# Kernel optimization log

Hardware: AMD Instinct MI355X
Metric: run time of the kernel (lower is better)

Reference implementation:

```python
import jax, jax.numpy as jnp
import numpy as np

N0, N1 = 20000, 20000     # users, items
F0 = 512                  # raw feature dim per type
HID = 64                  # hidden_dim == H * D
H, D = 8, 8               # num_heads, out_dim
P = 2                     # metapaths per side
E = 200000                # metapath instances per metapath
L = 3                     # metapath length (nodes)
B = 8192                  # link-prediction target batch
AV = 128                  # attn_vec_dim
CH = 128                  # ProductMLP hidden = max(128, HID//2)
ETYPES_USER = [[0, 1], [0, 1]]
ETYPES_ITEM = [[1, 0], [1, 0]]


def setup_inputs() -> dict:
    key = jax.random.key(0)
    ks = jax.random.split(key, 32)
    def nrm(k, shape, fan_in):
        return (jax.random.normal(k, shape, dtype=jnp.float32) * (1.414 / np.sqrt(fan_in))).astype(jnp.float32)
    inp = {}
    inp['feats0'] = jax.random.normal(ks[0], (N0, F0), dtype=jnp.float32)
    inp['feats1'] = jax.random.normal(ks[1], (N1, F0), dtype=jnp.float32)
    for t, off in ((0, 2), (1, 6)):
        inp[f'tower{t}_pw'] = nrm(ks[off], (F0, HID), F0)
        inp[f'tower{t}_pb'] = jnp.zeros((HID,), jnp.float32)
        inp[f'tower{t}_w2'] = nrm(ks[off + 1], (HID, HID), HID)
        inp[f'tower{t}_b2'] = jnp.zeros((HID,), jnp.float32)
        inp[f'tower{t}_g'] = jnp.ones((HID,), jnp.float32)
        inp[f'tower{t}_be'] = jnp.zeros((HID,), jnp.float32)
    inp['r_vec'] = jax.random.normal(ks[10], (2, HID // 2, 2), dtype=jnp.float32)
    inp['attn_user'] = nrm(ks[11], (P, H, D), D)
    inp['attn_item'] = nrm(ks[12], (P, H, D), D)
    inp['su_w1'] = nrm(ks[13], (HID, AV), HID)
    inp['su_b1'] = jnp.zeros((AV,), jnp.float32)
    inp['su_w2'] = nrm(ks[14], (AV,), AV)
    inp['si_w1'] = nrm(ks[15], (HID, AV), HID)
    inp['si_b1'] = jnp.zeros((AV,), jnp.float32)
    inp['si_w2'] = nrm(ks[16], (AV,), AV)
    inp['cw1'] = nrm(ks[17], (HID, CH), HID)
    inp['cb1'] = jnp.zeros((CH,), jnp.float32)
    inp['cw2'] = nrm(ks[18], (CH, 2), CH)
    inp['idx0'] = jnp.arange(N0, dtype=jnp.int32)
    inp['idx1'] = jnp.arange(N1, dtype=jnp.int32) + N0
    inp['emi_user'] = jax.random.randint(ks[20], (P, E, L), 0, N0 + N1, dtype=jnp.int32)
    inp['tgt_user'] = jax.random.randint(ks[21], (P, E), 0, B, dtype=jnp.int32)
    inp['emi_item'] = jax.random.randint(ks[22], (P, E, L), 0, N0 + N1, dtype=jnp.int32)
    inp['tgt_item'] = jax.random.randint(ks[23], (P, E), 0, B, dtype=jnp.int32)
    return inp


def _tower(x, pw, pb, w2, b2, g, be):
    # Linear -> GELU -> Linear -> residual -> LayerNorm (dropout off in eval)
    z = x @ pw + pb
    h = jax.nn.gelu(z, approximate=False)
    h = h @ w2 + b2
    y = h + z
    mu = y.mean(-1, keepdims=True)
    var = ((y - mu) ** 2).mean(-1, keepdims=True)
    return (y - mu) / jnp.sqrt(var + 1e-5) * g + be


def _rot_full(r_vec):
    # normalize to unit complex, then even etypes = r, odd etypes = conj(r)
    r = r_vec / jnp.linalg.norm(r_vec, axis=-1, keepdims=True)
    conj = r * jnp.array([1.0, -1.0], dtype=r.dtype)
    return jnp.stack([r, conj], axis=1).reshape(-1, r.shape[1], 2)  # [num_edge_type, HID//2, 2]


def _final_r(rfull, etypes):
    # cumulative complex rotation applied to each position along the metapath
    fr = [None] * L
    fr[L - 1] = jnp.stack([jnp.ones(HID // 2), jnp.zeros(HID // 2)], axis=1).astype(rfull.dtype)
    for i in range(L - 2, -1, -1):
        rv = rfull[etypes[i]]
        re = fr[i + 1][:, 0] * rv[:, 0] - fr[i + 1][:, 1] * rv[:, 1]
        im = fr[i + 1][:, 0] * rv[:, 1] + fr[i + 1][:, 1] * rv[:, 0]
        fr[i] = jnp.stack([re, im], axis=1)
    return jnp.stack(fr)  # [L, HID//2, 2]


def _metapath(feat, emi, tgt, attn, etypes, rfull):
    # gather node features along each metapath instance: [E, L, HID//2, 2]
    ed = feat[emi].reshape(emi.shape[0], L, HID // 2, 2)
    fr = _final_r(rfull, etypes)  # last position is identity rotation
    re = ed[..., 0] * fr[:, :, 0] - ed[..., 1] * fr[:, :, 1]
    im = ed[..., 0] * fr[:, :, 1] + ed[..., 1] * fr[:, :, 0]
    hidden = jnp.stack([re, im], -1).mean(axis=1).reshape(-1, HID)  # mean over metapath positions
    eft = hidden.reshape(-1, H, D)
    e = jax.nn.leaky_relu((eft * attn).sum(-1), 0.01)  # [E, H]
    # edge softmax over instances sharing a target node
    m = jax.ops.segment_max(e, tgt, num_segments=B)
    m = jnp.where(jnp.isfinite(m), m, 0.0)
    a = jnp.exp(e - m[tgt])
    s = jax.ops.segment_sum(a, tgt, num_segments=B)
    w = a / (s[tgt] + 1e-9)
    ret = jax.ops.segment_sum(w[..., None] * eft, tgt, num_segments=B)  # [B, H, D]
    return jax.nn.elu(ret.reshape(B, HID))


def _semantic(outs, w1, b1, w2):
    hs = jnp.stack(outs)  # [P, B, HID]
    s = (jnp.tanh(hs @ w1 + b1) @ w2).mean(axis=1)  # [P]
    beta = jax.nn.softmax(s)
    return (beta[:, None, None] * hs).sum(0)  # [B, HID]


def reference(feats0, feats1, tower0_pw, tower0_pb, tower0_w2, tower0_b2, tower0_g, tower0_be,
              tower1_pw, tower1_pb, tower1_w2, tower1_b2, tower1_g, tower1_be,
              r_vec, attn_user, attn_item, su_w1, su_b1, su_w2, si_w1, si_b1, si_w2,
              cw1, cb1, cw2, idx0, idx1, emi_user, tgt_user, emi_item, tgt_item):
    t0 = _tower(feats0, tower0_pw, tower0_pb, tower0_w2, tower0_b2, tower0_g, tower0_be)
    t1 = _tower(feats1, tower1_pw, tower1_pb, tower1_w2, tower1_b2, tower1_g, tower1_be)
    feat = jnp.zeros((N0 + N1, HID), jnp.float32).at[idx0].set(t0).at[idx1].set(t1)
    rfull = _rot_full(r_vec)
    user_outs = [_metapath(feat, emi_user[p], tgt_user[p], attn_user[p], ETYPES_USER[p], rfull) for p in range(P)]
    item_outs = [_metapath(feat, emi_item[p], tgt_item[p], attn_item[p], ETYPES_ITEM[p], rfull) for p in range(P)]
    h_user = _semantic(user_outs, su_w1, su_b1, su_w2)
    h_item = _semantic(item_outs, si_w1, si_b1, si_w2)
    x = h_user * h_item
    h = jax.nn.relu(x @ cw1 + cb1)
    logits = h @ cw2
    return jax.nn.softmax(logits, axis=-1)
```

## Files before the change

kernel.cpp:

```cpp
#include <hip/hip_runtime.h>
#include <hip/hip_bf16.h>
#include <math.h>

#define NN0 20000
#define NN1 20000
#define NTOT 40000
#define FF0 512
#define HIDD 64
#define EEE 200000
#define BBB 8192
#define AVV 128
#define CHH 128

typedef __bf16 bf16x8 __attribute__((ext_vector_type(8)));
typedef __bf16 bf16x4 __attribute__((ext_vector_type(4)));
typedef float f32x4 __attribute__((ext_vector_type(4)));
typedef float f32x2 __attribute__((ext_vector_type(2)));

__device__ __forceinline__ float fast_tanh(float x) {
    float e2 = __expf(2.f * x);
    return 1.f - 2.f / (e2 + 1.f);
}

__device__ __forceinline__ f32x2 bf2_to_f32x2(unsigned int c) {
    f32x2 r;
    r.x = __uint_as_float(c << 16);
    r.y = __uint_as_float(c & 0xffff0000u);
    return r;
}

__global__ __launch_bounds__(256) void prep_hist(
    const float* __restrict__ pw0, const float* __restrict__ pw1,
    const float* __restrict__ w20, const float* __restrict__ w21,
    __bf16* __restrict__ wprep, __bf16* __restrict__ w2prep,
    const int* __restrict__ tgt_user, const int* __restrict__ tgt_item,
    int* __restrict__ cnt)
{
    int bx = blockIdx.x;
    if (bx < 16) {
        int tw = bx & 1, seg = bx >> 1;
        const float* w = tw ? pw1 : pw0;
        __bf16* base = wprep + tw * 65536;
        for (int idx = seg * 4096 + threadIdx.x; idx < (seg + 1) * 4096; idx += 256) {
            int k = idx >> 6, n = idx & 63;
            float v = w[idx];
            __bf16 hi = (__bf16)v;
            __bf16 lo = (__bf16)(v - (float)hi);
            int ks = k >> 5, kb = (k >> 3) & 3, j = k & 7;
            int nt = n >> 4, fr = n & 15;
            int lane = kb * 16 + fr;
            int off = ((ks * 4 + nt) * 64 + lane) * 8 + j;
            base[off] = hi;
            base[32768 + off] = lo;
        }
        const float* w2 = tw ? w21 : w20;
        __bf16* base2 = w2prep + tw * 8192;
        for (int idx = seg * 512 + threadIdx.x; idx < (seg + 1) * 512; idx += 256) {
            int k = idx >> 6, n = idx & 63;
            float v = w2[idx];
            __bf16 hi = (__bf16)v;
            __bf16 lo = (__bf16)(v - (float)hi);
            int ks = k >> 5, kb = (k >> 3) & 3, j = k & 7;
            int nt = n >> 4, fr = n & 15;
            int lane = kb * 16 + fr;
            int off = ((ks * 4 + nt) * 64 + lane) * 8 + j;
            base2[off] = hi;
            base2[4096 + off] = lo;
        }
    } else {
        int flat = bx - 16;
        int combo = flat & 3, blk = flat >> 2;
        const int* tgt = (combo < 2 ? tgt_user : tgt_item) + (long)(combo & 1) * EEE;
        int i = blk * 256 + threadIdx.x;
        if (i < EEE) atomicAdd(&cnt[combo * BBB + tgt[i]], 1);
    }
}

__global__ __launch_bounds__(256) void scan_kernel(const int* __restrict__ cnt, int* __restrict__ offs,
                                                   int* __restrict__ cur32, float* __restrict__ s_acc)
{
    int pth = blockIdx.x;
    if (pth == 0 && threadIdx.x < 4) s_acc[threadIdx.x] = 0.f;
    const int* c = cnt + pth * BBB;
    int* o = offs + pth * (BBB + 1);
    __shared__ int part[256];
    int tid = threadIdx.x;
    int base = tid * 32;
    int local[32];
    int sum = 0;
    for (int j = 0; j < 32; j++) { local[j] = sum; sum += c[base + j]; }
    part[tid] = sum;
    __syncthreads();
    for (int d = 1; d < 256; d <<= 1) {
        int v = (tid >= d) ? part[tid - d] : 0;
        __syncthreads();
        part[tid] += v;
        __syncthreads();
    }
    int pre = (tid == 0) ? 0 : part[tid - 1];
    for (int j = 0; j < 32; j++) {
        int val = pre + local[j];
        o[base + j] = val;
        if (((base + j) & 255) == 0) cur32[pth * 32 + ((base + j) >> 8)] = val;
    }
    if (tid == 255) o[BBB] = pre + sum;
}

#define CHUNKF 512
__global__ __launch_bounds__(64) void tower_binA(
    const float* __restrict__ x0, const float* __restrict__ x1,
    const __bf16* __restrict__ wprep, const __bf16* __restrict__ w2prep,
    const float* __restrict__ pb0, const float* __restrict__ pb1,
    const float* __restrict__ b20, const float* __restrict__ b21,
    const float* __restrict__ g0, const float* __restrict__ g1,
    const float* __restrict__ be0, const float* __restrict__ be1,
    const int* __restrict__ idxa, const int* __restrict__ idxb,
    __hip_bfloat16* __restrict__ feat,
    const int* __restrict__ tgt_user, const int* __restrict__ tgt_item,
    const int* __restrict__ emi_user, const int* __restrict__ emi_item,
    int* __restrict__ cur32, ushort4* __restrict__ binbuf)
{
    __shared__ __align__(16) char pool[4624];
    int bx = blockIdx.x;
    if (bx < 2500) {
        int tile = bx >> 1, tw = bx & 1;
        const float* x  = tw ? x1 : x0;
        const float* pb = tw ? pb1 : pb0;
        const float* b2 = tw ? b21 : b20;
        const float* g  = tw ? g1 : g0;
        const float* be = tw ? be1 : be0;
        const int* idx  = tw ? idxb : idxa;
        float (*hs)[68] = (float(*)[68])pool;

        int l = threadIdx.x;
        int fr = l & 15, kb = l >> 4;
        int row0 = tile * 16;
        const float* xp = x + (long)(row0 + fr) * FF0 + kb * 8;
        const __bf16* bp = wprep + tw * 65536;

        f32x4 acc[4];
#pragma unroll
        for (int nt = 0; nt < 4; nt++) acc[nt] = (f32x4){0.f, 0.f, 0.f, 0.f};

        float4 a0c, a1c, a0n, a1n;
        bf16x8 bhc[4], blc[4], bhn[4], bln[4];

        a0c = *(const float4*)xp;
        a1c = *(const float4*)(xp + 4);
#pragma unroll
        for (int nt = 0; nt < 4; nt++) {
            bhc[nt] = *(const bf16x8*)(bp + (nt * 64 + l) * 8);
            blc[nt] = *(const bf16x8*)(bp + 32768 + (nt * 64 + l) * 8);
        }

#pragma unroll 2
        for (int ks = 0; ks < 16; ks++) {
            if (ks + 1 < 16) {
                a0n = *(const float4*)(xp + (ks + 1) * 32);
                a1n = *(const float4*)(xp + (ks + 1) * 32 + 4);
#pragma unroll
                for (int nt = 0; nt < 4; nt++) {
                    bhn[nt] = *(const bf16x8*)(bp + (((ks + 1) * 4 + nt) * 64 + l) * 8);
                    bln[nt] = *(const bf16x8*)(bp + 32768 + (((ks + 1) * 4 + nt) * 64 + l) * 8);
                }
            }
            float av[8] = {a0c.x, a0c.y, a0c.z, a0c.w, a1c.x, a1c.y, a1c.z, a1c.w};
            bf16x8 ah, al;
#pragma unroll
            for (int j = 0; j < 8; j++) {
                __bf16 h = (__bf16)av[j];
                ah[j] = h;
                al[j] = (__bf16)(av[j] - (float)h);
            }
#pragma unroll
            for (int nt = 0; nt < 4; nt++) {
                acc[nt] = __builtin_amdgcn_mfma_f32_16x16x32_bf16(ah, bhc[nt], acc[nt], 0, 0, 0);
                acc[nt] = __builtin_amdgcn_mfma_f32_16x16x32_bf16(al, bhc[nt], acc[nt], 0, 0, 0);
                acc[nt] = __builtin_amdgcn_mfma_f32_16x16x32_bf16(ah, blc[nt], acc[nt], 0, 0, 0);
            }
            a0c = a0n; a1c = a1n;
#pragma unroll
            for (int nt = 0; nt < 4; nt++) { bhc[nt] = bhn[nt]; blc[nt] = bln[nt]; }
        }

        float pbv[4], b2v[4];
#pragma unroll
        for (int nt = 0; nt < 4; nt++) { pbv[nt] = pb[nt * 16 + fr]; b2v[nt] = b2[nt * 16 + fr]; }
        f32x4 acc2[4];
#pragma unroll
        for (int nt = 0; nt < 4; nt++) {
#pragma unroll
            for (int j = 0; j < 4; j++) {
                float z = acc[nt][j] + pbv[nt];
                float h = 0.5f * z * (1.f + erff(z * 0.70710678118654752f));
                hs[kb * 4 + j][nt * 16 + fr] = h;
                acc2[nt][j] = z + b2v[nt];
            }
        }
        __syncthreads();

        const __bf16* w2p = w2prep + tw * 8192;
#pragma unroll
        for (int ks = 0; ks < 2; ks++) {
            float4 h0 = *(const float4*)&hs[fr][ks * 32 + kb * 8];
            float4 h1 = *(const float4*)&hs[fr][ks * 32 + kb * 8 + 4];
            float hv[8] = {h0.x, h0.y, h0.z, h0.w, h1.x, h1.y, h1.z, h1.w};
            bf16x8 ah, al;
#pragma unroll
            for (int j = 0; j < 8; j++) {
                __bf16 h = (__bf16)hv[j];
                ah[j] = h;
                al[j] = (__bf16)(hv[j] - (float)h);
            }
#pragma unroll
            for (int nt = 0; nt < 4; nt++) {
                bf16x8 bh2 = *(const bf16x8*)(w2p + ((ks * 4 + nt) * 64 + l) * 8);
                bf16x8 bl2 = *(const bf16x8*)(w2p + 4096 + ((ks * 4 + nt) * 64 + l) * 8);
                acc2[nt] = __builtin_amdgcn_mfma_f32_16x16x32_bf16(ah, bh2, acc2[nt], 0, 0, 0);
                acc2[nt] = __builtin_amdgcn_mfma_f32_16x16x32_bf16(al, bh2, acc2[nt], 0, 0, 0);
                acc2[nt] = __builtin_amdgcn_mfma_f32_16x16x32_bf16(ah, bl2, acc2[nt], 0, 0, 0);
            }
        }
        __syncthreads();

        float gv[4], bev[4];
#pragma unroll
        for (int nt = 0; nt < 4; nt++) { gv[nt] = g[nt * 16 + fr]; bev[nt] = be[nt * 16 + fr]; }
#pragma unroll
        for (int j = 0; j < 4; j++) {
            float p = acc2[0][j] + acc2[1][j] + acc2[2][j] + acc2[3][j];
            p += __shfl_xor(p, 1); p += __shfl_xor(p, 2);
            p += __shfl_xor(p, 4); p += __shfl_xor(p, 8);
            float mu = p * (1.f / 64.f);
            float d[4], vs = 0.f;
#pragma unroll
            for (int nt = 0; nt < 4; nt++) { d[nt] = acc2[nt][j] - mu; vs += d[nt] * d[nt]; }
            vs += __shfl_xor(vs, 1); vs += __shfl_xor(vs, 2);
            vs += __shfl_xor(vs, 4); vs += __shfl_xor(vs, 8);
            float is = 1.f / sqrtf(vs * (1.f / 64.f) + 1e-5f);
#pragma unroll
            for (int nt = 0; nt < 4; nt++)
                hs[kb * 4 + j][nt * 16 + fr] = d[nt] * is * gv[nt] + bev[nt];
        }
        __syncthreads();
#pragma unroll 4
        for (int r = 0; r < 16; r++) {
            int grow = row0 + r;
            feat[(long)idx[grow] * HIDD + l] = __float2bfloat16(hs[r][l]);
        }
    } else {
        int flat = bx - 2500;
        int combo = flat & 3;
        int base = (flat >> 2) * CHUNKF;
        const int* tgt = (combo < 2 ? tgt_user : tgt_item) + (long)(combo & 1) * EEE;
        const int* emi = (combo < 2 ? emi_user : emi_item) + (long)(combo & 1) * EEE * 3;
        ushort4* sbuf = (ushort4*)pool;
        int* lcnt  = (int*)(pool + 4096);
        int* lofs  = lcnt + 32;
        int* gbase = lofs + 33;
        int* lcur  = gbase + 32;
        int tid = threadIdx.x;
        if (tid < 32) { lcnt[tid] = 0; lcur[tid] = 0; }
        __syncthreads();
        ushort4 ent[8]; int bk[8];
#pragma unroll
        for (int ps = 0; ps < 8; ps++) {
            int i = base + ps * 64 + tid;
            if (i < EEE) {
                int t = tgt[i];
                ent[ps] = make_ushort4((unsigned short)emi[3 * i], (unsigned short)emi[3 * i + 1],
                                       (unsigned short)emi[3 * i + 2], (unsigned short)t);
                bk[ps] = t >> 8;
                atomicAdd(&lcnt[bk[ps]], 1);
            } else bk[ps] = -1;
        }
        __syncthreads();
        if (tid == 0) {
            int run = 0;
            for (int k = 0; k < 32; k++) { lofs[k] = run; run += lcnt[k]; }
            lofs[32] = run;
        }
        __syncthreads();
        if (tid < 32) gbase[tid] = atomicAdd(&cur32[combo * 32 + tid], lcnt[tid]);
        __syncthreads();
#pragma unroll
        for (int ps = 0; ps < 8; ps++) {
            if (bk[ps] >= 0) {
                int pos = lofs[bk[ps]] + atomicAdd(&lcur[bk[ps]], 1);
                sbuf[pos] = ent[ps];
            }
        }
        __syncthreads();
        int total = lofs[32];
        ushort4* dst = binbuf + (long)combo * EEE;
        for (int j = tid; j < total; j += 64) {
            ushort4 e = sbuf[j];
            int k = e.w >> 8;
            dst[gbase[k] + (j - lofs[k])] = e;
        }
    }
}

__global__ __launch_bounds__(256) void binB_kernel(
    const int* __restrict__ offs, int* __restrict__ cur,
    const ushort4* __restrict__ binbuf, ushort4* __restrict__ nodes)
{
    int combo = blockIdx.y;
    int k = blockIdx.x >> 1, part = blockIdx.x & 1;
    const int* of = offs + combo * (BBB + 1);
    int rbeg = of[k << 8], rend = of[(k + 1) << 8];
    const ushort4* src = binbuf + (long)combo * EEE;
    ushort4* dst = nodes + (long)combo * EEE;
    int* cu = cur + combo * BBB;
    for (int j = rbeg + part * 256 + threadIdx.x; j < rend; j += 512) {
        ushort4 e = src[j];
        int t = e.w;
        int pos = of[t] + atomicAdd(&cu[t], 1);
        dst[pos] = e;
    }
}

__global__ __launch_bounds__(256) void flash_mp(
    const __hip_bfloat16* __restrict__ feat, const ushort4* __restrict__ nodes,
    const int* __restrict__ offs, const float* __restrict__ r_vec,
    const float* __restrict__ attn_user, const float* __restrict__ attn_item,
    float* __restrict__ ret)
{
    int combo = blockIdx.y;
    int wid = threadIdx.x >> 6, lane = threadIdx.x & 63;
    int half = lane >> 5, p = lane & 31;
    int side = combo >> 1;
    const float* attn = (side == 0 ? attn_user : attn_item) + (combo & 1) * 64;
    const unsigned int* f2 = (const unsigned int*)feat;
    float2 rb = ((const float2*)r_vec)[p];
    float invn = 1.f / sqrtf(rb.x * rb.x + rb.y * rb.y);
    float rvx = rb.x * invn, rvy = rb.y * invn;
    if (side == 0) rvy = -rvy;
    float aRe = attn[2 * p], aIm = attn[2 * p + 1];
    f32x2 av  = { aRe * (1.f / 3.f), aIm * (1.f / 3.f) };
    f32x2 apv = { (rvx * aRe + rvy * aIm) * (1.f / 3.f),
                  (rvx * aIm - rvy * aRe) * (1.f / 3.f) };
    int t = blockIdx.x * 4 + wid;
    const int* of = offs + combo * (BBB + 1);
    int beg = of[t], end = of[t + 1];
    int n = end - beg;
    const ushort4* nd = nodes + (long)combo * EEE;

    float m = -3.4e38f, s = 0.f;
    f32x2 A02 = {0.f, 0.f}, A1 = {0.f, 0.f};

    unsigned int c0[4], c1[4], c2[4];
    ushort4 nq[4];
    if (n > 0) {
#pragma unroll
        for (int q = 0; q < 4; q++) {
            ushort4 a = nd[min(beg + 2 * q + half, EEE - 1)];
            c0[q] = f2[(int)a.x * 32 + p];
            c1[q] = f2[(int)a.y * 32 + p];
            c2[q] = f2[(int)a.z * 32 + p];
        }
#pragma unroll
        for (int q = 0; q < 4; q++)
            nq[q] = nd[min(beg + 8 + 2 * q + half, EEE - 1)];
    }
    for (int it = 0; it < n; it += 8) {
        f32x2 u1[4], v02[4];
        float e[4];
#pragma unroll
        for (int q = 0; q < 4; q++) {
            f32x2 u0 = bf2_to_f32x2(c0[q]);
            u1[q]    = bf2_to_f32x2(c1[q]);
            f32x2 u2 = bf2_to_f32x2(c2[q]);
            v02[q] = u0 + u2;
        }
        if (it + 8 < n) {
#pragma unroll
            for (int q = 0; q < 4; q++) {
                c0[q] = f2[(int)nq[q].x * 32 + p];
                c1[q] = f2[(int)nq[q].y * 32 + p];
                c2[q] = f2[(int)nq[q].z * 32 + p];
            }
#pragma unroll
            for (int q = 0; q < 4; q++)
                nq[q] = nd[min(beg + it + 16 + 2 * q + half, EEE - 1)];
        }
#pragma unroll
        for (int q = 0; q < 4; q++) {
            f32x2 tt = v02[q] * av + u1[q] * apv;
            float pa = tt.x + tt.y;
            pa += __shfl_xor(pa, 1);
            pa += __shfl_xor(pa, 2);
            e[q] = fmaxf(pa, 0.01f * pa);
        }
        if (it + 8 > n) {
#pragma unroll
            for (int q = 0; q < 4; q++)
                if (it + 2 * q + half >= n) e[q] = -3.4e38f;
        }
        float mx = fmaxf(fmaxf(e[0], e[1]), fmaxf(e[2], e[3]));
        float mn = fmaxf(m, fmaxf(mx, __shfl_xor(mx, 32)));
        float alpha = __expf(m - mn);
        s *= alpha; A02 *= alpha; A1 *= alpha;
        float wl = 0.f;
#pragma unroll
        for (int q = 0; q < 4; q++) {
            float w = __expf(e[q] - mn);
            wl += w;
            A02 += v02[q] * w;
            A1  += u1[q] * w;
        }
        s += wl + __shfl_xor(wl, 32);
        m = mn;
    }
    float Sx = A02.x + __shfl_xor(A02.x, 32);
    float Sy = A02.y + __shfl_xor(A02.y, 32);
    float Tx = A1.x + __shfl_xor(A1.x, 32);
    float Ty = A1.y + __shfl_xor(A1.y, 32);
    float inv = (1.f / 3.f) / (s + 1e-9f);
    float vx = (Sx + rvx * Tx - rvy * Ty) * inv;
    float vy = (Sy + rvx * Ty + rvy * Tx) * inv;
    vx = vx > 0.f ? vx : __expf(vx) - 1.f;
    vy = vy > 0.f ? vy : __expf(vy) - 1.f;
    if (half == 0)
        ((float2*)ret)[((long)combo * BBB + t) * 32 + p] = make_float2(vx, vy);
}

__global__ __launch_bounds__(256) void sem_kernel(
    const float* __restrict__ ret,
    const float* __restrict__ su_w1, const float* __restrict__ su_b1, const float* __restrict__ su_w2,
    const float* __restrict__ si_w1, const float* __restrict__ si_b1, const float* __restrict__ si_w2,
    float* __restrict__ s_acc)
{
    int combo = blockIdx.y;
    int side = combo >> 1;
    const float* w1 = side ? si_w1 : su_w1;
    const float* b1 = side ? si_b1 : su_b1;
    const float* w2 = side ? si_w2 : su_w2;
    __shared__ float vs[64][68];
    __shared__ float w1s[64][128];
    int tid = threadIdx.x;
    int rowbase = blockIdx.x * 64;
    const float4* r4 = (const float4*)ret;
    for (int li = tid; li < 1024; li += 256) {
        int r = li >> 4, c4 = li & 15;
        float4 v = r4[((long)combo * BBB + rowbase + r) * 16 + c4];
        *(float4*)&vs[r][c4 * 4] = v;
    }
    const float4* w14 = (const float4*)w1;
    for (int li = tid; li < 2048; li += 256) {
        float4 v = w14[li];
        *(float4*)&w1s[li >> 5][(li & 31) * 4] = v;
    }
    __syncthreads();
    int ct = tid & 15, rt = tid >> 4;
    float acc[4][8];
#pragma unroll
    for (int cc = 0; cc < 8; cc++) {
        float b = b1[8 * ct + cc];
#pragma unroll
        for (int j = 0; j < 4; j++) acc[j][cc] = b;
    }
    for (int k = 0; k < 64; k += 4) {
        float4 xv[4];
#pragma unroll
        for (int j = 0; j < 4; j++) xv[j] = *(const float4*)&vs[4 * rt + j][k];
#pragma unroll
        for (int kk = 0; kk < 4; kk++) {
            float4 wv0 = *(const float4*)&w1s[k + kk][8 * ct];
            float4 wv1 = *(const float4*)&w1s[k + kk][8 * ct + 4];
#pragma unroll
            for (int j = 0; j < 4; j++) {
                float xx = kk == 0 ? xv[j].x : kk == 1 ? xv[j].y : kk == 2 ? xv[j].z : xv[j].w;
                acc[j][0] = fmaf(xx, wv0.x, acc[j][0]);
                acc[j][1] = fmaf(xx, wv0.y, acc[j][1]);
                acc[j][2] = fmaf(xx, wv0.z, acc[j][2]);
                acc[j][3] = fmaf(xx, wv0.w, acc[j][3]);
                acc[j][4] = fmaf(xx, wv1.x, acc[j][4]);
                acc[j][5] = fmaf(xx, wv1.y, acc[j][5]);
                acc[j][6] = fmaf(xx, wv1.z, acc[j][6]);
                acc[j][7] = fmaf(xx, wv1.w, acc[j][7]);
            }
        }
    }
    float tot = 0.f;
#pragma unroll
    for (int cc = 0; cc < 8; cc++) {
        float w2v = w2[8 * ct + cc];
#pragma unroll
        for (int j = 0; j < 4; j++) tot += fast_tanh(acc[j][cc]) * w2v;
    }
    for (int off = 32; off; off >>= 1) tot += __shfl_xor(tot, off);
    __shared__ float red[4];
    int lane = tid & 63, wid = tid >> 6;
    if (lane == 0) red[wid] = tot;
    __syncthreads();
    if (tid == 0) atomicAdd(&s_acc[combo], red[0] + red[1] + red[2] + red[3]);
}

__global__ __launch_bounds__(256) void final_kernel(
    const float* __restrict__ ret, const float* __restrict__ s_acc,
    const float* __restrict__ cw1, const float* __restrict__ cb1, const float* __restrict__ cw2,
    float* __restrict__ outp)
{
    float s0 = s_acc[0] * (1.f / BBB), s1 = s_acc[1] * (1.f / BBB);
    float s2 = s_acc[2] * (1.f / BBB), s3 = s_acc[3] * (1.f / BBB);
    float mu = fmaxf(s0, s1);
    float e0 = __expf(s0 - mu), e1 = __expf(s1 - mu);
    float bu0 = e0 / (e0 + e1), bu1 = e1 / (e0 + e1);
    float mi = fmaxf(s2, s3);
    float f0 = __expf(s2 - mi), f1 = __expf(s3 - mi);
    float bi0 = f0 / (f0 + f1), bi1 = f1 / (f0 + f1);

    __shared__ float xsld[64][68];
    __shared__ float w1s[64][128];
    int tid = threadIdx.x;
    int rowbase = blockIdx.x * 64;
    const float4* r4 = (const float4*)ret;
    for (int li = tid; li < 1024; li += 256) {
        int r = li >> 4, c4 = li & 15;
        float4 a = r4[((long)0 * BBB + rowbase + r) * 16 + c4];
        float4 b = r4[((long)1 * BBB + rowbase + r) * 16 + c4];
        float4 cc = r4[((long)2 * BBB + rowbase + r) * 16 + c4];
        float4 d = r4[((long)3 * BBB + rowbase + r) * 16 + c4];
        float4 xv;
        xv.x = (bu0 * a.x + bu1 * b.x) * (bi0 * cc.x + bi1 * d.x);
        xv.y = (bu0 * a.y + bu1 * b.y) * (bi0 * cc.y + bi1 * d.y);
        xv.z = (bu0 * a.z + bu1 * b.z) * (bi0 * cc.z + bi1 * d.z);
        xv.w = (bu0 * a.w + bu1 * b.w) * (bi0 * cc.w + bi1 * d.w);
        *(float4*)&xsld[r][c4 * 4] = xv;
    }
    const float4* w14 = (const float4*)cw1;
    for (int li = tid; li < 2048; li += 256) {
        float4 v = w14[li];
        *(float4*)&w1s[li >> 5][(li & 31) * 4] = v;
    }
    __syncthreads();
    int ct = tid & 15, rt = tid >> 4;
    float acc[4][8];
#pragma unroll
    for (int cc = 0; cc < 8; cc++) {
        float b = cb1[8 * ct + cc];
#pragma unroll
        for (int j = 0; j < 4; j++) acc[j][cc] = b;
    }
    for (int k = 0; k < 64; k += 4) {
        float4 xv[4];
#pragma unroll
        for (int j = 0; j < 4; j++) xv[j] = *(const float4*)&xsld[4 * rt + j][k];
#pragma unroll
        for (int kk = 0; kk < 4; kk++) {
            float4 wv0 = *(const float4*)&w1s[k + kk][8 * ct];
            float4 wv1 = *(const float4*)&w1s[k + kk][8 * ct + 4];
#pragma unroll
            for (int j = 0; j < 4; j++) {
                float xx = kk == 0 ? xv[j].x : kk == 1 ? xv[j].y : kk == 2 ? xv[j].z : xv[j].w;
                acc[j][0] = fmaf(xx, wv0.x, acc[j][0]);
                acc[j][1] = fmaf(xx, wv0.y, acc[j][1]);
                acc[j][2] = fmaf(xx, wv0.z, acc[j][2]);
                acc[j][3] = fmaf(xx, wv0.w, acc[j][3]);
                acc[j][4] = fmaf(xx, wv1.x, acc[j][4]);
                acc[j][5] = fmaf(xx, wv1.y, acc[j][5]);
                acc[j][6] = fmaf(xx, wv1.z, acc[j][6]);
                acc[j][7] = fmaf(xx, wv1.w, acc[j][7]);
            }
        }
    }
    float pp0[4], pp1[4];
#pragma unroll
    for (int j = 0; j < 4; j++) { pp0[j] = 0.f; pp1[j] = 0.f; }
#pragma unroll
    for (int cc = 0; cc < 8; cc++) {
        int col = 8 * ct + cc;
        float c0 = cw2[col * 2], c1 = cw2[col * 2 + 1];
#pragma unroll
        for (int j = 0; j < 4; j++) {
            float h = fmaxf(acc[j][cc], 0.f);
            pp0[j] = fmaf(h, c0, pp0[j]);
            pp1[j] = fmaf(h, c1, pp1[j]);
        }
    }
    __syncthreads();
    float2* red = (float2*)xsld;
#pragma unroll
    for (int j = 0; j < 4; j++)
        red[(4 * rt + j) * 16 + ct] = make_float2(pp0[j], pp1[j]);
    __syncthreads();
    if (tid < 64) {
        float q0 = 0.f, q1 = 0.f;
        for (int i = 0; i < 16; i++) {
            float2 e = red[tid * 16 + i];
            q0 += e.x; q1 += e.y;
        }
        float mx = fmaxf(q0, q1);
        float a0 = __expf(q0 - mx), a1 = __expf(q1 - mx);
        float dn = a0 + a1;
        outp[(rowbase + tid) * 2] = a0 / dn;
        outp[(rowbase + tid) * 2 + 1] = a1 / dn;
    }
}

extern "C" void kernel_launch(void* const* d_in, const int* in_sizes, int n_in,
                              void* d_out, int out_size, void* d_ws, size_t ws_size,
                              hipStream_t stream)
{
    const float* feats0 = (const float*)d_in[0];
    const float* feats1 = (const float*)d_in[1];
    const float* t0_pw = (const float*)d_in[2];
    const float* t0_pb = (const float*)d_in[3];
    const float* t0_w2 = (const float*)d_in[4];
    const float* t0_b2 = (const float*)d_in[5];
    const float* t0_g  = (const float*)d_in[6];
    const float* t0_be = (const float*)d_in[7];
    const float* t1_pw = (const float*)d_in[8];
    const float* t1_pb = (const float*)d_in[9];
    const float* t1_w2 = (const float*)d_in[10];
    const float* t1_b2 = (const float*)d_in[11];
    const float* t1_g  = (const float*)d_in[12];
    const float* t1_be = (const float*)d_in[13];
    const float* r_vec = (const float*)d_in[14];
    const float* attn_user = (const float*)d_in[15];
    const float* attn_item = (const float*)d_in[16];
    const float* su_w1 = (const float*)d_in[17];
    const float* su_b1 = (const float*)d_in[18];
    const float* su_w2 = (const float*)d_in[19];
    const float* si_w1 = (const float*)d_in[20];
    const float* si_b1 = (const float*)d_in[21];
    const float* si_w2 = (const float*)d_in[22];
    const float* cw1 = (const float*)d_in[23];
    const float* cb1 = (const float*)d_in[24];
    const float* cw2 = (const float*)d_in[25];
    const int* idx0 = (const int*)d_in[26];
    const int* idx1 = (const int*)d_in[27];
    const int* emi_user = (const int*)d_in[28];
    const int* tgt_user = (const int*)d_in[29];
    const int* emi_item = (const int*)d_in[30];
    const int* tgt_item = (const int*)d_in[31];
    float* outp = (float*)d_out;

    char* ws = (char*)d_ws;
    __hip_bfloat16* feat = (__hip_bfloat16*)(ws + 0);
    int*     cnt    = (int*)(ws + 5120000);
    int*     cur    = (int*)(ws + 5251072);
    int*     cur32  = (int*)(ws + 5382144);
    int*     offs   = (int*)(ws + 5382656);
    float*   s_acc  = (float*)(ws + 5513984);
    ushort4* binbuf = (ushort4*)(ws + 5514240);
    ushort4* nodes  = (ushort4*)(ws + 11914240);
    float*   ret_buf= (float*)(ws + 18314240);
    __bf16*  wprep  = (__bf16*)(ws + 26702848);
    __bf16*  w2prep = (__bf16*)(ws + 11914240);

    hipMemsetAsync(cnt, 0, 2 * 4 * BBB * sizeof(int), stream);

    prep_hist<<<16 + 4 * ((EEE + 255) / 256), 256, 0, stream>>>(
        t0_pw, t1_pw, t0_w2, t1_w2, wprep, w2prep, tgt_user, tgt_item, cnt);

    scan_kernel<<<4, 256, 0, stream>>>(cnt, offs, cur32, s_acc);

    tower_binA<<<2500 + 4 * ((EEE + CHUNKF - 1) / CHUNKF), 64, 0, stream>>>(
        feats0, feats1, wprep, w2prep, t0_pb, t1_pb,
        t0_b2, t1_b2, t0_g, t1_g, t0_be, t1_be, idx0, idx1, feat,
        tgt_user, tgt_item, emi_user, emi_item, cur32, binbuf);

    binB_kernel<<<dim3(64, 4), 256, 0, stream>>>(offs, cur, binbuf, nodes);

    flash_mp<<<dim3(BBB / 4, 4), 256, 0, stream>>>(feat, nodes, offs, r_vec,
                                                   attn_user, attn_item, ret_buf);

    sem_kernel<<<dim3(BBB / 64, 4), 256, 0, stream>>>(ret_buf, su_w1, su_b1, su_w2,
                                                      si_w1, si_b1, si_w2, s_acc);
    final_kernel<<<BBB / 64, 256, 0, stream>>>(ret_buf, s_acc, cw1, cb1, cw2, outp);
}
```

Before: 332.6 us.

## Split tower tile across two waves per block and widen binning chunks

The fused tower/binning kernel now launches 128-thread blocks. In the tower path, each wave computes half of the 64 output columns for its 16-row tile, and the LayerNorm mean and variance are combined across the two waves through shared-memory partial sums. The binning path processes 1024-entry chunks with 128 threads, so that path launches half as many blocks. The aim is more parallelism and less per-wave latency on the x-streaming GEMM. In exchange it adds extra barriers and LDS traffic, and each wave re-reads the same A rows from memory.

```diff
diff --git a/kernel.cpp b/kernel.cpp
--- a/kernel.cpp
+++ b/kernel.cpp
@@ -106,8 +106,8 @@
     if (tid == 255) o[BBB] = pre + sum;
 }
 
-#define CHUNKF 512
-__global__ __launch_bounds__(64) void tower_binA(
+#define CHUNKF 1024
+__global__ __launch_bounds__(128) void tower_binA(
     const float* __restrict__ x0, const float* __restrict__ x1,
     const __bf16* __restrict__ wprep, const __bf16* __restrict__ w2prep,
     const float* __restrict__ pb0, const float* __restrict__ pb1,
@@ -120,7 +120,7 @@
     const int* __restrict__ emi_user, const int* __restrict__ emi_item,
     int* __restrict__ cur32, ushort4* __restrict__ binbuf)
 {
-    __shared__ __align__(16) char pool[4624];
+    __shared__ __align__(16) char pool[8960];
     int bx = blockIdx.x;
     if (bx < 2500) {
         int tile = bx >> 1, tw = bx & 1;
@@ -131,26 +131,30 @@
         const float* be = tw ? be1 : be0;
         const int* idx  = tw ? idxb : idxa;
         float (*hs)[68] = (float(*)[68])pool;
-
-        int l = threadIdx.x;
+        float* pq  = (float*)(pool + 4352);
+        float* pq2 = (float*)(pool + 4480);
+
+        int wv = threadIdx.x >> 6;
+        int l = threadIdx.x & 63;
         int fr = l & 15, kb = l >> 4;
+        int nt0 = 2 * wv;
         int row0 = tile * 16;
         const float* xp = x + (long)(row0 + fr) * FF0 + kb * 8;
         const __bf16* bp = wprep + tw * 65536;
 
-        f32x4 acc[4];
-#pragma unroll
-        for (int nt = 0; nt < 4; nt++) acc[nt] = (f32x4){0.f, 0.f, 0.f, 0.f};
+        f32x4 acc[2];
+#pragma unroll
+        for (int n2 = 0; n2 < 2; n2++) acc[n2] = (f32x4){0.f, 0.f, 0.f, 0.f};
 
         float4 a0c, a1c, a0n, a1n;
-        bf16x8 bhc[4], blc[4], bhn[4], bln[4];
+        bf16x8 bhc[2], blc[2], bhn[2], bln[2];
 
         a0c = *(const float4*)xp;
         a1c = *(const float4*)(xp + 4);
 #pragma unroll
-        for (int nt = 0; nt < 4; nt++) {
-            bhc[nt] = *(const bf16x8*)(bp + (nt * 64 + l) * 8);
-            blc[nt] = *(const bf16x8*)(bp + 32768 + (nt * 64 + l) * 8);
+        for (int n2 = 0; n2 < 2; n2++) {
+            bhc[n2] = *(const bf16x8*)(bp + ((nt0 + n2) * 64 + l) * 8);
+            blc[n2] = *(const bf16x8*)(bp + 32768 + ((nt0 + n2) * 64 + l) * 8);
         }
 
 #pragma unroll 2
@@ -159,9 +163,9 @@
                 a0n = *(const float4*)(xp + (ks + 1) * 32);
                 a1n = *(const float4*)(xp + (ks + 1) * 32 + 4);
 #pragma unroll
-                for (int nt = 0; nt < 4; nt++) {
-                    bhn[nt] = *(const bf16x8*)(bp + (((ks + 1) * 4 + nt) * 64 + l) * 8);
-                    bln[nt] = *(const bf16x8*)(bp + 32768 + (((ks + 1) * 4 + nt) * 64 + l) * 8);
+                for (int n2 = 0; n2 < 2; n2++) {
+                    bhn[n2] = *(const bf16x8*)(bp + (((ks + 1) * 4 + nt0 + n2) * 64 + l) * 8);
+                    bln[n2] = *(const bf16x8*)(bp + 32768 + (((ks + 1) * 4 + nt0 + n2) * 64 + l) * 8);
                 }
             }
             float av[8] = {a0c.x, a0c.y, a0c.z, a0c.w, a1c.x, a1c.y, a1c.z, a1c.w};
@@ -173,28 +177,31 @@
                 al[j] = (__bf16)(av[j] - (float)h);
             }
 #pragma unroll
-            for (int nt = 0; nt < 4; nt++) {
-                acc[nt] = __builtin_amdgcn_mfma_f32_16x16x32_bf16(ah, bhc[nt], acc[nt], 0, 0, 0);
-                acc[nt] = __builtin_amdgcn_mfma_f32_16x16x32_bf16(al, bhc[nt], acc[nt], 0, 0, 0);
-                acc[nt] = __builtin_amdgcn_mfma_f32_16x16x32_bf16(ah, blc[nt], acc[nt], 0, 0, 0);
+            for (int n2 = 0; n2 < 2; n2++) {
+                acc[n2] = __builtin_amdgcn_mfma_f32_16x16x32_bf16(ah, bhc[n2], acc[n2], 0, 0, 0);
+                acc[n2] = __builtin_amdgcn_mfma_f32_16x16x32_bf16(al, bhc[n2], acc[n2], 0, 0, 0);
+                acc[n2] = __builtin_amdgcn_mfma_f32_16x16x32_bf16(ah, blc[n2], acc[n2], 0, 0, 0);
             }
             a0c = a0n; a1c = a1n;
 #pragma unroll
-            for (int nt = 0; nt < 4; nt++) { bhc[nt] = bhn[nt]; blc[nt] = bln[nt]; }
-        }
-
-        float pbv[4], b2v[4];
-#pragma unroll
-        for (int nt = 0; nt < 4; nt++) { pbv[nt] = pb[nt * 16 + fr]; b2v[nt] = b2[nt * 16 + fr]; }
-        f32x4 acc2[4];
-#pragma unroll
-        for (int nt = 0; nt < 4; nt++) {
+            for (int n2 = 0; n2 < 2; n2++) { bhc[n2] = bhn[n2]; blc[n2] = bln[n2]; }
+        }
+
+        float pbv[2], b2v[2];
+#pragma unroll
+        for (int n2 = 0; n2 < 2; n2++) {
+            pbv[n2] = pb[(nt0 + n2) * 16 + fr];
+            b2v[n2] = b2[(nt0 + n2) * 16 + fr];
+        }
+        f32x4 acc2[2];
+#pragma unroll
+        for (int n2 = 0; n2 < 2; n2++) {
 #pragma unroll
             for (int j = 0; j < 4; j++) {
-                float z = acc[nt][j] + pbv[nt];
+                float z = acc[n2][j] + pbv[n2];
                 float h = 0.5f * z * (1.f + erff(z * 0.70710678118654752f));
-                hs[kb * 4 + j][nt * 16 + fr] = h;
-                acc2[nt][j] = z + b2v[nt];
+                hs[kb * 4 + j][(nt0 + n2) * 16 + fr] = h;
+                acc2[n2][j] = z + b2v[n2];
             }
         }
         __syncthreads();
@@ -213,40 +220,66 @@
                 al[j] = (__bf16)(hv[j] - (float)h);
             }
 #pragma unroll
-            for (int nt = 0; nt < 4; nt++) {
-                bf16x8 bh2 = *(const bf16x8*)(w2p + ((ks * 4 + nt) * 64 + l) * 8);
-                bf16x8 bl2 = *(const bf16x8*)(w2p + 4096 + ((ks * 4 + nt) * 64 + l) * 8);
-                acc2[nt] = __builtin_amdgcn_mfma_f32_16x16x32_bf16(ah, bh2, acc2[nt], 0, 0, 0);
-                acc2[nt] = __builtin_amdgcn_mfma_f32_16x16x32_bf16(al, bh2, acc2[nt], 0, 0, 0);
-                acc2[nt] = __builtin_amdgcn_mfma_f32_16x16x32_bf16(ah, bl2, acc2[nt], 0, 0, 0);
-            }
-        }
-        __syncthreads();
-
-        float gv[4], bev[4];
-#pragma unroll
-        for (int nt = 0; nt < 4; nt++) { gv[nt] = g[nt * 16 + fr]; bev[nt] = be[nt * 16 + fr]; }
+            for (int n2 = 0; n2 < 2; n2++) {
+                bf16x8 bh2 = *(const bf16x8*)(w2p + ((ks * 4 + nt0 + n2) * 64 + l) * 8);
+                bf16x8 bl2 = *(const bf16x8*)(w2p + 4096 + ((ks * 4 + nt0 + n2) * 64 + l) * 8);
+                acc2[n2] = __builtin_amdgcn_mfma_f32_16x16x32_bf16(ah, bh2, acc2[n2], 0, 0, 0);
+                acc2[n2] = __builtin_amdgcn_mfma_f32_16x16x32_bf16(al, bh2, acc2[n2], 0, 0, 0);
+                acc2[n2] = __builtin_amdgcn_mfma_f32_16x16x32_bf16(ah, bl2, acc2[n2], 0, 0, 0);
+            }
+        }
+
+        float pj[4];
 #pragma unroll
         for (int j = 0; j < 4; j++) {
-            float p = acc2[0][j] + acc2[1][j] + acc2[2][j] + acc2[3][j];
+            float p = acc2[0][j] + acc2[1][j];
             p += __shfl_xor(p, 1); p += __shfl_xor(p, 2);
             p += __shfl_xor(p, 4); p += __shfl_xor(p, 8);
-            float mu = p * (1.f / 64.f);
-            float d[4], vs = 0.f;
-#pragma unroll
-            for (int nt = 0; nt < 4; nt++) { d[nt] = acc2[nt][j] - mu; vs += d[nt] * d[nt]; }
-            vs += __shfl_xor(vs, 1); vs += __shfl_xor(vs, 2);
-            vs += __shfl_xor(vs, 4); vs += __shfl_xor(vs, 8);
-            float is = 1.f / sqrtf(vs * (1.f / 64.f) + 1e-5f);
-#pragma unroll
-            for (int nt = 0; nt < 4; nt++)
-                hs[kb * 4 + j][nt * 16 + fr] = d[nt] * is * gv[nt] + bev[nt];
-        }
-        __syncthreads();
-#pragma unroll 4
-        for (int r = 0; r < 16; r++) {
-            int grow = row0 + r;
-            feat[(long)idx[grow] * HIDD + l] = __float2bfloat16(hs[r][l]);
+            pj[j] = p;
+        }
+        if (fr == 0) {
+#pragma unroll
+            for (int j = 0; j < 4; j++) pq[wv * 16 + kb * 4 + j] = pj[j];
+        }
+        __syncthreads();
+        float mu[4];
+#pragma unroll
+        for (int j = 0; j < 4; j++)
+            mu[j] = (pj[j] + pq[(wv ^ 1) * 16 + kb * 4 + j]) * (1.f / 64.f);
+        float d[2][4], vj[4];
+#pragma unroll
+        for (int j = 0; j < 4; j++) {
+            d[0][j] = acc2[0][j] - mu[j];
+            d[1][j] = acc2[1][j] - mu[j];
+            float v = d[0][j] * d[0][j] + d[1][j] * d[1][j];
+            v += __shfl_xor(v, 1); v += __shfl_xor(v, 2);
+            v += __shfl_xor(v, 4); v += __shfl_xor(v, 8);
+            vj[j] = v;
+        }
+        if (fr == 0) {
+#pragma unroll
+            for (int j = 0; j < 4; j++) pq2[wv * 16 + kb * 4 + j] = vj[j];
+        }
+        __syncthreads();
+        float gv[2], bev[2];
+#pragma unroll
+        for (int n2 = 0; n2 < 2; n2++) {
+            gv[n2] = g[(nt0 + n2) * 16 + fr];
+            bev[n2] = be[(nt0 + n2) * 16 + fr];
+        }
+#pragma unroll
+        for (int j = 0; j < 4; j++) {
+            float var = (vj[j] + pq2[(wv ^ 1) * 16 + kb * 4 + j]) * (1.f / 64.f);
+            float is = 1.f / sqrtf(var + 1e-5f);
+#pragma unroll
+            for (int n2 = 0; n2 < 2; n2++)
+                hs[kb * 4 + j][(nt0 + n2) * 16 + fr] = d[n2][j] * is * gv[n2] + bev[n2];
+        }
+        __syncthreads();
+#pragma unroll
+        for (int r = 0; r < 8; r++) {
+            int rr = wv * 8 + r;
+            feat[(long)idx[row0 + rr] * HIDD + l] = __float2bfloat16(hs[rr][l]);
         }
     } else {
         int flat = bx - 2500;
@@ -255,7 +288,7 @@
         const int* tgt = (combo < 2 ? tgt_user : tgt_item) + (long)(combo & 1) * EEE;
         const int* emi = (combo < 2 ? emi_user : emi_item) + (long)(combo & 1) * EEE * 3;
         ushort4* sbuf = (ushort4*)pool;
-        int* lcnt  = (int*)(pool + 4096);
+        int* lcnt  = (int*)(pool + 8192);
         int* lofs  = lcnt + 32;
         int* gbase = lofs + 33;
         int* lcur  = gbase + 32;
@@ -265,7 +298,7 @@
         ushort4 ent[8]; int bk[8];
 #pragma unroll
         for (int ps = 0; ps < 8; ps++) {
-            int i = base + ps * 64 + tid;
+            int i = base + ps * 128 + tid;
             if (i < EEE) {
                 int t = tgt[i];
                 ent[ps] = make_ushort4((unsigned short)emi[3 * i], (unsigned short)emi[3 * i + 1],
@@ -293,7 +326,7 @@
         __syncthreads();
         int total = lofs[32];
         ushort4* dst = binbuf + (long)combo * EEE;
-        for (int j = tid; j < total; j += 64) {
+        for (int j = tid; j < total; j += 128) {
             ushort4 e = sbuf[j];
             int k = e.w >> 8;
             dst[gbase[k] + (j - lofs[k])] = e;
@@ -657,7 +690,7 @@
 
     scan_kernel<<<4, 256, 0, stream>>>(cnt, offs, cur32, s_acc);
 
-    tower_binA<<<2500 + 4 * ((EEE + CHUNKF - 1) / CHUNKF), 64, 0, stream>>>(
+    tower_binA<<<2500 + 4 * ((EEE + CHUNKF - 1) / CHUNKF), 128, 0, stream>>>(
         feats0, feats1, wprep, w2prep, t0_pb, t1_pb,
         t0_b2, t1_b2, t0_g, t1_g, t0_be, t1_be, idx0, idx1, feat,
         tgt_user, tgt_item, emi_user, emi_item, cur32, binbuf);
```

New measurement: 333.5 us. About the same (+0.3%).
